# Kernel optimization log

Hardware: AMD Instinct MI355X
Metric: run time of the kernel (lower is better)

## Reference

```python
import jax, jax.numpy as jnp
import numpy as np
from jax import lax

B, N, D, E, P, K, H = 32, 512, 512, 8, 96, 25, 4
PAD = 12  # conv padding so length is preserved


def setup_inputs() -> dict:
    key = jax.random.key(0)
    ks = jax.random.split(key, 16)
    s = 0.05  # weight scale to keep softmax/cosine well-conditioned
    x = jax.random.normal(ks[0], (B, N, D), dtype=jnp.float32)
    router = jax.random.normal(ks[1], (1, E, D), dtype=jnp.float32)
    Wq = jax.random.normal(ks[2], (D, D), dtype=jnp.float32) * s
    bq = jax.random.normal(ks[3], (D,), dtype=jnp.float32) * s
    Wk = jax.random.normal(ks[4], (D, D), dtype=jnp.float32) * s
    bk = jax.random.normal(ks[5], (D,), dtype=jnp.float32) * s
    Wv = jax.random.normal(ks[6], (D, D), dtype=jnp.float32) * s
    bv = jax.random.normal(ks[7], (D,), dtype=jnp.float32) * s
    Wo = jax.random.normal(ks[8], (D, D), dtype=jnp.float32) * s
    bo = jax.random.normal(ks[9], (D,), dtype=jnp.float32) * s
    Wc = jax.random.normal(ks[10], (E, 2, K), dtype=jnp.float32) * s  # E experts' Conv1d(2,1,25) stacked as out-channels
    bc = jax.random.normal(ks[11], (E,), dtype=jnp.float32) * s
    Wp = jax.random.normal(ks[12], (E, D, P), dtype=jnp.float32) * s  # E experts' Linear(D,P), stored (in,out)
    bp = jax.random.normal(ks[13], (E, P), dtype=jnp.float32) * s
    return {"x": x, "router": router, "Wq": Wq, "bq": bq, "Wk": Wk, "bk": bk,
            "Wv": Wv, "bv": bv, "Wo": Wo, "bo": bo, "Wc": Wc, "bc": bc,
            "Wp": Wp, "bp": bp}


def _forward(x, router, Wq, bq, Wk, bk, Wv, bv, Wo, bo, Wc, bc, Wp, bp):
    b, n, d = x.shape
    e = router.shape[1]
    dk = d // H
    r = jnp.broadcast_to(router, (b, e, d))
    # multi-head attention: queries=router slots, keys/values=x (dropout = identity at eval)
    q = (r @ Wq + bq).reshape(b, e, H, dk)
    k = (x @ Wk + bk).reshape(b, n, H, dk)
    v = (x @ Wv + bv).reshape(b, n, H, dk)
    scale = 1.0 / jnp.sqrt(jnp.asarray(dk, x.dtype))
    scores = jnp.einsum('blhe,bshe->bhls', q, k)  # [b,H,e,n]
    A = jax.nn.softmax(scale * scores, axis=-1)
    att = jnp.einsum('bhls,bshd->blhd', A, v).reshape(b, e, d)
    att = att @ Wo + bo  # [b,e,d]
    # cosine-similarity routing score, mapped to (1+pi)/2
    dot = jnp.einsum('bed,bnd->ben', att, x)
    norm_a = jnp.linalg.norm(att, axis=2, keepdims=True)          # [b,e,1]
    norm_x = jnp.linalg.norm(x, axis=2)[:, None, :]                # [b,1,n]
    score = (1.0 + dot / (norm_a * norm_x)) / 2.0                  # [b,e,n]
    idx = jnp.argmax(score, axis=1)                                # [b,n] expert per token
    z = jnp.take_along_axis(att, idx[:, :, None], axis=1)          # [b,n,d]
    result = jnp.stack([x, z], axis=-2).reshape(b * n, 2, d)       # [bn,2,d]
    # run all E expert convs at once (experts stacked as output channels)
    conv_out = lax.conv_general_dilated(
        result, Wc, window_strides=(1,), padding=[(PAD, PAD)],
        dimension_numbers=('NCH', 'OIH', 'NCH')) + bc[None, :, None]  # [bn,E,d]
    lin = jnp.einsum('nel,elp->nep', conv_out, Wp) + bp[None]         # [bn,E,P]
    flat_idx = idx.reshape(-1)
    out = jnp.take_along_axis(lin, flat_idx[:, None, None], axis=1)[:, 0, :]
    return out.reshape(b, n, P)


def reference(x, router, Wq, bq, Wk, bk, Wv, bv, Wo, bo, Wc, bc, Wp, bp):
    return _forward(x, router, Wq, bq, Wk, bk, Wv, bv, Wo, bo, Wc, bc, Wp, bp)
```

## Files before the change

### kernel.cpp

```cpp
#include <hip/hip_runtime.h>
#include <hip/hip_bf16.h>

#define B_ 32
#define N_ 512
#define D_ 512
#define E_ 8
#define P_ 96
#define KC 25
#define H_ 4
#define DK 128
#define HE 32
#define BN 16384

typedef short short8 __attribute__((ext_vector_type(8)));
typedef float f32x4 __attribute__((ext_vector_type(4)));

#define OCNT  4096
#define OS2   4352
#define OM    5120
#define OC    21504
#define OA    21536
#define OAP   545824
#define OATT  676896
#define OTOK  807968
#define OWEFF 939040
#define OZC   1332256
#define OUP   1356832
#define OA1   5551136

__device__ __forceinline__ float b2f(short s) {
  unsigned u = ((unsigned)(unsigned short)s) << 16;
  return __builtin_bit_cast(float, u);
}
__device__ __forceinline__ unsigned short f2b(float f) {
  return __builtin_bit_cast(unsigned short, __float2bfloat16(f));
}

__global__ __launch_bounds__(256) void k_head(const float* __restrict__ router,
        const float* __restrict__ Wq, const float* __restrict__ bq,
        const float* __restrict__ Wk, const float* __restrict__ bk,
        const float* __restrict__ Wp, const float* __restrict__ Wc,
        float* __restrict__ M, float* __restrict__ c,
        int* __restrict__ cnt, float* __restrict__ s2,
        __hip_bfloat16* __restrict__ weff) {
  __shared__ float sm[5824];
  int bid = blockIdx.x;
  int tid = threadIdx.x;
  if (bid < 64) {
    float* rs = sm;
    float* ps = sm + 512;
    float* qs = sm + 768;
    int he = bid >> 1, ch = bid & 1;
    int h = he >> 3, e = he & 7;
    for (int i = tid; i < 512; i += 256) rs[i] = router[e * D_ + i];
    __syncthreads();
    {
      int j = tid & 127, dh = tid >> 7;
      const float* wq = Wq + h * 128 + j;
      float acc = 0.f;
      for (int d = dh * 256; d < dh * 256 + 256; d += 4) {
        acc = fmaf(rs[d], wq[d * D_], acc);
        acc = fmaf(rs[d + 1], wq[(d + 1) * D_], acc);
        acc = fmaf(rs[d + 2], wq[(d + 2) * D_], acc);
        acc = fmaf(rs[d + 3], wq[(d + 3) * D_], acc);
      }
      ps[dh * 128 + j] = acc;
    }
    __syncthreads();
    if (tid < 128) qs[tid] = ps[tid] + ps[128 + tid] + bq[h * 128 + tid];
    __syncthreads();
    {
      int d0 = ch * 256 + tid;
      const float* wrow = Wk + d0 * D_ + h * 128;
      float acc = 0.f;
      for (int jj = 0; jj < 128; jj += 4) {
        float4 wv = *(const float4*)(wrow + jj);
        acc = fmaf(wv.x, qs[jj], acc);
        acc = fmaf(wv.y, qs[jj + 1], acc);
        acc = fmaf(wv.z, qs[jj + 2], acc);
        acc = fmaf(wv.w, qs[jj + 3], acc);
      }
      M[he * D_ + d0] = acc;
    }
    if (ch == 0 && tid < 64) {
      float s = qs[tid] * bk[h * 128 + tid] + qs[tid + 64] * bk[h * 128 + tid + 64];
#pragma unroll
      for (int off = 32; off; off >>= 1) s += __shfl_xor(s, off);
      if (tid == 0) c[he] = s;
    }
  } else if (bid < 192) {
    float* T = sm;
    float* wcs = sm + 5760;
    int eb = bid - 64;
    int e = eb >> 4, mc = eb & 15;
    int lo = mc * 32 - 12;
    for (int idx = tid; idx < 56 * 24; idx += 256) {
      int lp = idx / 24, p4 = (idx - lp * 24) * 4;
      int l = lo + lp;
      float4 v = {0.f, 0.f, 0.f, 0.f};
      if (l >= 0 && l < D_) v = *(const float4*)(Wp + (e * D_ + l) * P_ + p4);
      T[p4 * 60 + lp] = v.x; T[(p4 + 1) * 60 + lp] = v.y;
      T[(p4 + 2) * 60 + lp] = v.z; T[(p4 + 3) * 60 + lp] = v.w;
    }
    if (tid < 50) wcs[tid] = Wc[e * 2 * KC + tid];
    __syncthreads();
    int m = tid & 31, pg = tid >> 5;
#pragma unroll
    for (int j = 0; j < 2; ++j)
      for (int k2 = 0; k2 < 12; ++k2) {
        int p = pg * 12 + k2;
        float acc = 0.f;
#pragma unroll
        for (int k = 0; k < KC; ++k)
          acc = fmaf(wcs[j * 25 + k], T[p * 60 + m - k + 24], acc);
        weff[(((e * 2 + j) * P_ + p) << 9) + mc * 32 + m] = __float2bfloat16(acc);
      }
  } else {
    int e = bid - 192;
    if (bid == 192) cnt[tid] = 0;
    if (tid < 192) {
      int p = tid % 96, lg = tid / 96;
      float s = 0.f;
      const float* wp = Wp + e * D_ * P_ + p;
      for (int l = lg * 256; l < lg * 256 + 256; ++l) s += wp[l * P_];
      sm[lg * 96 + p] = s;
    }
    __syncthreads();
    if (tid < 96) s2[e * 96 + tid] = sm[tid] + sm[96 + tid];
  }
}

__global__ __launch_bounds__(128) void k_logits(const float* __restrict__ x,
        const float* __restrict__ M, float* __restrict__ A0,
        float* __restrict__ A1) {
  __shared__ float xs[64 * 132];
  __shared__ float Ms[32 * 132];
  int dh = blockIdx.x & 1;
  int nt8 = (blockIdx.x >> 1) & 7;
  int b = blockIdx.x >> 4;
  int tid = threadIdx.x;
  const float* xb = x + (b * N_ + nt8 * 64) * D_ + dh * 256;
  const float* Mb = M + dh * 256;
  float acc[4][4] = {{0.f}};
  for (int kc = 0; kc < 2; ++kc) {
    for (int idx = tid; idx < 2048; idx += 128) {
      int r = idx >> 5, c4 = (idx & 31) * 4;
      *(float4*)(xs + r * 132 + c4) = *(const float4*)(xb + r * D_ + kc * 128 + c4);
    }
    for (int idx = tid; idx < 1024; idx += 128) {
      int r = idx >> 5, c4 = (idx & 31) * 4;
      *(float4*)(Ms + r * 132 + c4) = *(const float4*)(Mb + r * D_ + kc * 128 + c4);
    }
    __syncthreads();
    int nt = tid & 15, ht = tid >> 4;
#pragma unroll 4
    for (int d4 = 0; d4 < 128; d4 += 4) {
      float4 xv[4], mv[4];
#pragma unroll
      for (int i = 0; i < 4; ++i)
        xv[i] = *(const float4*)(xs + (nt + 16 * i) * 132 + d4);
#pragma unroll
      for (int j = 0; j < 4; ++j)
        mv[j] = *(const float4*)(Ms + (ht + 8 * j) * 132 + d4);
#pragma unroll
      for (int i = 0; i < 4; ++i)
#pragma unroll
        for (int j = 0; j < 4; ++j) {
          float s = acc[i][j];
          s = fmaf(xv[i].x, mv[j].x, s);
          s = fmaf(xv[i].y, mv[j].y, s);
          s = fmaf(xv[i].z, mv[j].z, s);
          s = fmaf(xv[i].w, mv[j].w, s);
          acc[i][j] = s;
        }
    }
    __syncthreads();
  }
  int nt = tid & 15, ht = tid >> 4;
  float* Ad = dh ? A1 : A0;
#pragma unroll
  for (int j = 0; j < 4; ++j) {
    int he = ht + 8 * j;
#pragma unroll
    for (int i = 0; i < 4; ++i)
      Ad[(b * HE + he) * N_ + nt8 * 64 + nt + 16 * i] = acc[i][j];
  }
}

__global__ __launch_bounds__(512) void k_usm(const float* __restrict__ x,
        const float* __restrict__ A0, const float* __restrict__ A1,
        const float* __restrict__ c, float* __restrict__ up) {
  __shared__ float V[32 * 520];
  __shared__ float As[64 * 33];
  __shared__ float inv_s[32];
  int nq = blockIdx.x, b = blockIdx.y;
  int tid = threadIdx.x;
  const float scale = 0.08838834764831845f;
  for (int idx = tid; idx < 32 * 128; idx += 512) {
    int he = idx >> 7, n4 = (idx & 127) * 4;
    float4 a0 = *(const float4*)(A0 + (b * HE + he) * N_ + n4);
    float4 a1 = *(const float4*)(A1 + (b * HE + he) * N_ + n4);
    float cc = c[he];
    float4 v;
    v.x = scale * (a0.x + a1.x + cc);
    v.y = scale * (a0.y + a1.y + cc);
    v.z = scale * (a0.z + a1.z + cc);
    v.w = scale * (a0.w + a1.w + cc);
    *(float4*)(V + he * 520 + n4) = v;
  }
  __syncthreads();
  {
    int w = tid >> 6, lane = tid & 63;
    int he = w * 4 + (lane >> 4);
    int l16 = lane & 15;
    float* vr = V + he * 520;
    float m = -1e30f;
    for (int n = l16; n < 512; n += 16) m = fmaxf(m, vr[n]);
    m = fmaxf(m, __shfl_xor(m, 1)); m = fmaxf(m, __shfl_xor(m, 2));
    m = fmaxf(m, __shfl_xor(m, 4)); m = fmaxf(m, __shfl_xor(m, 8));
    float s = 0.f;
    for (int n = l16; n < 512; n += 16) {
      float e = expf(vr[n] - m);
      vr[n] = e;
      s += e;
    }
    s += __shfl_xor(s, 1); s += __shfl_xor(s, 2);
    s += __shfl_xor(s, 4); s += __shfl_xor(s, 8);
    if (l16 == 0) inv_s[he] = 1.0f / s;
  }
  __syncthreads();
  for (int idx = tid; idx < 64 * 32; idx += 512) {
    int n = idx & 63, he = idx >> 6;
    As[n * 33 + he] = V[he * 520 + nq * 64 + n] * inv_s[he];
  }
  __syncthreads();
  int dq = tid & 127, hg = tid >> 7;
  const float* xb = x + (b * N_ + nq * 64) * D_ + dq * 4;
  float acc[8][4];
#pragma unroll
  for (int j = 0; j < 8; ++j)
#pragma unroll
    for (int k = 0; k < 4; ++k) acc[j][k] = 0.f;
  for (int n = 0; n < 64; ++n) {
    float4 xv = *(const float4*)(xb + n * D_);
    const float* ar = As + n * 33 + hg * 8;
#pragma unroll
    for (int j = 0; j < 8; ++j) {
      float a = ar[j];
      acc[j][0] = fmaf(a, xv.x, acc[j][0]);
      acc[j][1] = fmaf(a, xv.y, acc[j][1]);
      acc[j][2] = fmaf(a, xv.z, acc[j][2]);
      acc[j][3] = fmaf(a, xv.w, acc[j][3]);
    }
  }
  float* o = up + (((b * 8 + nq) * HE) + hg * 8) * D_ + dq * 4;
#pragma unroll
  for (int j = 0; j < 8; ++j) {
    float4 v; v.x = acc[j][0]; v.y = acc[j][1]; v.z = acc[j][2]; v.w = acc[j][3];
    *(float4*)(o + j * D_) = v;
  }
}

__global__ __launch_bounds__(256) void k_attpre(const float* __restrict__ up,
        const float* __restrict__ Wv, const float* __restrict__ bv,
        float* __restrict__ ap) {
  __shared__ float us[8 * D_];
  int e = blockIdx.x & 7;
  int ic = (blockIdx.x >> 3) & 3;
  int bq = blockIdx.x >> 5;
  for (int idx = threadIdx.x; idx < 8 * 128; idx += 256) {
    int rr = idx >> 7, d4 = (idx & 127) * 4;
    const float* base = up + (((bq * 8 + rr) * 8) * HE + ic * 8 + e) * D_ + d4;
    float4 s = {0.f, 0.f, 0.f, 0.f};
#pragma unroll
    for (int nq = 0; nq < 8; ++nq) {
      float4 v = *(const float4*)(base + nq * HE * D_);
      s.x += v.x; s.y += v.y; s.z += v.z; s.w += v.w;
    }
    *(float4*)(us + rr * D_ + d4) = s;
  }
  __syncthreads();
  int i = ic * 128 + (threadIdx.x & 127);
  int bg = threadIdx.x >> 7;
  const float* usb = us + bg * 4 * D_;
  float acc[4] = {0.f, 0.f, 0.f, 0.f};
  for (int d = 0; d < D_; d += 4) {
    float w0 = Wv[(d + 0) * D_ + i];
    float w1 = Wv[(d + 1) * D_ + i];
    float w2 = Wv[(d + 2) * D_ + i];
    float w3 = Wv[(d + 3) * D_ + i];
#pragma unroll
    for (int r = 0; r < 4; ++r) {
      float4 uv = *(const float4*)(usb + r * D_ + d);
      float s = acc[r];
      s = fmaf(uv.x, w0, s); s = fmaf(uv.y, w1, s);
      s = fmaf(uv.z, w2, s); s = fmaf(uv.w, w3, s);
      acc[r] = s;
    }
  }
  float bvi = bv[i];
#pragma unroll
  for (int r = 0; r < 4; ++r)
    ap[((bq * 8 + bg * 4 + r) * E_ + e) * D_ + i] = acc[r] + bvi;
}

__global__ __launch_bounds__(256) void k_att(const float* __restrict__ ap,
        const float* __restrict__ Wo, const float* __restrict__ bo,
        float* __restrict__ att) {
  __shared__ float ps[8 * D_];
  int b = blockIdx.x >> 2, oc = blockIdx.x & 3;
  for (int idx = threadIdx.x; idx < 8 * D_; idx += 256)
    ps[idx] = ap[b * E_ * D_ + idx];
  __syncthreads();
  int o = oc * 128 + (threadIdx.x & 127);
  int eg = threadIdx.x >> 7;
  const float* pe = ps + eg * 4 * D_;
  float acc[4] = {0.f, 0.f, 0.f, 0.f};
  for (int i2 = 0; i2 < D_; i2 += 4) {
    float w0 = Wo[(i2 + 0) * D_ + o];
    float w1 = Wo[(i2 + 1) * D_ + o];
    float w2 = Wo[(i2 + 2) * D_ + o];
    float w3 = Wo[(i2 + 3) * D_ + o];
#pragma unroll
    for (int r = 0; r < 4; ++r) {
      float4 pv = *(const float4*)(pe + r * D_ + i2);
      float s = acc[r];
      s = fmaf(pv.x, w0, s); s = fmaf(pv.y, w1, s);
      s = fmaf(pv.z, w2, s); s = fmaf(pv.w, w3, s);
      acc[r] = s;
    }
  }
  float boo = bo[o];
#pragma unroll
  for (int r = 0; r < 4; ++r)
    att[(b * E_ + eg * 4 + r) * D_ + o] = acc[r] + boo;
}

__global__ __launch_bounds__(256) void k_route2(const float* __restrict__ x,
        const float* __restrict__ att, const __hip_bfloat16* __restrict__ weff,
        const float* __restrict__ s2, const float* __restrict__ bc,
        const float* __restrict__ bp, int* __restrict__ cnt,
        int* __restrict__ tok, float* __restrict__ zc) {
  __shared__ float att_s[8 * D_];
  __shared__ float rn[8];
  __shared__ float red[4][520];
  __shared__ int blist[8][32];
  __shared__ int bcnt[8];
  int b = blockIdx.x >> 4, tile = blockIdx.x & 15;
  for (int idx = threadIdx.x; idx < 1024; idx += 256)
    *(float4*)(att_s + idx * 4) = *(const float4*)(att + b * E_ * D_ + idx * 4);
  if (threadIdx.x < 8) bcnt[threadIdx.x] = 0;
  __syncthreads();
  {
    int e = threadIdx.x >> 5, l = threadIdx.x & 31;
    float s = 0.f;
    for (int d0 = l; d0 < D_; d0 += 32) {
      float v = att_s[e * D_ + d0];
      s = fmaf(v, v, s);
    }
#pragma unroll
    for (int off = 16; off; off >>= 1) s += __shfl_xor(s, off);
    if (l == 0) rn[e] = 1.0f / sqrtf(s);
  }
  __syncthreads();
  int w = threadIdx.x >> 6, lane = threadIdx.x & 63;
  int e2 = lane & 7, ch = lane >> 3;
  float* rw = red[w];
  for (int i = 0; i < 8; ++i) {
    int t = b * N_ + tile * 32 + w * 8 + i;
    const float* xp = x + t * D_ + lane * 8;
    float4 xa = *(const float4*)xp;
    float4 xb4 = *(const float4*)(xp + 4);
    float p[8];
#pragma unroll
    for (int e = 0; e < 8; ++e) {
      const float* apt = att_s + e * D_ + lane * 8;
      float4 a0 = *(const float4*)apt;
      float4 a1 = *(const float4*)(apt + 4);
      float s = a0.x * xa.x;
      s = fmaf(a0.y, xa.y, s); s = fmaf(a0.z, xa.z, s); s = fmaf(a0.w, xa.w, s);
      s = fmaf(a1.x, xb4.x, s); s = fmaf(a1.y, xb4.y, s);
      s = fmaf(a1.z, xb4.z, s); s = fmaf(a1.w, xb4.w, s);
      p[e] = s;
    }
#pragma unroll
    for (int e = 0; e < 8; ++e) rw[e * 65 + lane] = p[e];
    float s = 0.f;
#pragma unroll
    for (int k = 0; k < 8; ++k) s += rw[e2 * 65 + ch * 8 + k];
    s += __shfl_xor(s, 8); s += __shfl_xor(s, 16); s += __shfl_xor(s, 32);
    float sc = s * rn[e2];
    int be = e2;
#pragma unroll
    for (int off = 1; off < 8; off <<= 1) {
      float o = __shfl_xor(sc, off);
      int oe = __shfl_xor(be, off);
      if (o > sc || (o == sc && oe < be)) { sc = o; be = oe; }
    }
    if (lane == 0) {
      int slot = atomicAdd(&bcnt[be], 1);
      blist[be][slot] = t;
    }
  }
  __syncthreads();
  {
    int e = threadIdx.x >> 5, r = threadIdx.x & 31;
    int ce = bcnt[e];
    int gs = 0;
    if (r == 0 && ce > 0) gs = atomicAdd(&cnt[e * 32], ce);
    gs = __shfl(gs, (threadIdx.x & 63) & 32);
    for (int k2 = r; k2 < ce; k2 += 32) tok[e * BN + gs + k2] = blist[e][k2];
  }
  int grp = threadIdx.x >> 4, l16 = threadIdx.x & 15;
  for (int r = 0; r < 3; ++r) {
    int P = tile * 48 + r * 16 + grp;
    int ez = P / 96, p = P - ez * 96;
    const short* wrow = (const short*)weff + (((ez * 2 + 1) * P_ + p) << 9);
    const float* arow = att_s + ez * D_;
    float acc = 0.f;
#pragma unroll
    for (int seg = 0; seg < 4; ++seg) {
      int d = seg * 128 + l16 * 8;
      short8 w8 = *(const short8*)(wrow + d);
      const float* a8 = arow + d;
      acc = fmaf(a8[0], b2f(w8[0]), acc); acc = fmaf(a8[1], b2f(w8[1]), acc);
      acc = fmaf(a8[2], b2f(w8[2]), acc); acc = fmaf(a8[3], b2f(w8[3]), acc);
      acc = fmaf(a8[4], b2f(w8[4]), acc); acc = fmaf(a8[5], b2f(w8[5]), acc);
      acc = fmaf(a8[6], b2f(w8[6]), acc); acc = fmaf(a8[7], b2f(w8[7]), acc);
    }
    acc += __shfl_xor(acc, 1); acc += __shfl_xor(acc, 2);
    acc += __shfl_xor(acc, 4); acc += __shfl_xor(acc, 8);
    if (l16 == 0)
      zc[(b * E_ + ez) * P_ + p] = acc + bc[ez] * s2[ez * 96 + p] + bp[ez * 96 + p];
  }
}

__global__ __launch_bounds__(256) void k_final(const float* __restrict__ x,
        const __hip_bfloat16* __restrict__ weff, const float* __restrict__ zc,
        const int* __restrict__ cnt, const int* __restrict__ tok,
        float* __restrict__ out) {
  __shared__ __align__(16) unsigned short xsb[32 * 520];
  __shared__ int toks[32];
  int g = blockIdx.x;
  int cl_e[E_], bs[E_ + 1];
  bs[0] = 0;
#pragma unroll
  for (int e = 0; e < E_; ++e) {
    cl_e[e] = cnt[e * 32];
    bs[e + 1] = bs[e] + ((cl_e[e] + 31) >> 5);
  }
  if (g >= bs[E_]) return;
  int e = 0;
#pragma unroll
  for (int k = 1; k < E_; ++k) if (g >= bs[k]) e = k;
  int base = (g - bs[e]) * 32;
  int cnt_e = cl_e[e];
  int cl = cnt_e - base; if (cl > 32) cl = 32;
  int tid = threadIdx.x;
  if (tid < 32) toks[tid] = (tid < cl) ? tok[e * BN + base + tid] : tok[e * BN + base];
  __syncthreads();
  for (int idx = tid; idx < 32 * 128; idx += 256) {
    int r = idx >> 7, c4 = (idx & 127) * 4;
    float4 v = *(const float4*)(x + toks[r] * D_ + c4);
    ushort4 u4;
    u4.x = f2b(v.x); u4.y = f2b(v.y); u4.z = f2b(v.z); u4.w = f2b(v.w);
    *(ushort4*)(xsb + r * 520 + c4) = u4;
  }
  __syncthreads();
  int wave = tid >> 6, lane = tid & 63;
  int mw = wave & 1, nw = wave >> 1;
  int m16 = lane & 15, quad = lane >> 4;
  const short* w0 = (const short*)(weff + (e * 2 + 0) * P_ * D_);
  f32x4 acc[3];
#pragma unroll
  for (int nt = 0; nt < 3; ++nt) acc[nt] = (f32x4){0.f, 0.f, 0.f, 0.f};
  const short* arow = (const short*)xsb + (mw * 16 + m16) * 520 + quad * 8;
  const short* brow = w0 + (nw * 48 + m16) * D_ + quad * 8;
  for (int kt = 0; kt < 16; ++kt) {
    int koff = kt * 32;
    short8 a = *(const short8*)(arow + koff);
#pragma unroll
    for (int nt = 0; nt < 3; ++nt) {
      short8 bf = *(const short8*)(brow + nt * 16 * D_ + koff);
      acc[nt] = __builtin_amdgcn_mfma_f32_16x16x32_bf16(a, bf, acc[nt], 0, 0, 0);
    }
  }
#pragma unroll
  for (int nt = 0; nt < 3; ++nt)
#pragma unroll
    for (int rr = 0; rr < 4; ++rr) {
      int row = mw * 16 + quad * 4 + rr;
      if (row < cl) {
        int tg = toks[row];
        int bb = tg >> 9;
        int p = nw * 48 + nt * 16 + m16;
        out[tg * P_ + p] = acc[nt][rr] + zc[(bb * E_ + e) * P_ + p];
      }
    }
}

extern "C" void kernel_launch(void* const* d_in, const int* in_sizes, int n_in,
                              void* d_out, int out_size, void* d_ws, size_t ws_size,
                              hipStream_t stream) {
  const float* x      = (const float*)d_in[0];
  const float* router = (const float*)d_in[1];
  const float* Wq     = (const float*)d_in[2];
  const float* bq     = (const float*)d_in[3];
  const float* Wk     = (const float*)d_in[4];
  const float* bk     = (const float*)d_in[5];
  const float* Wv     = (const float*)d_in[6];
  const float* bv     = (const float*)d_in[7];
  const float* Wo     = (const float*)d_in[8];
  const float* bo     = (const float*)d_in[9];
  const float* Wc     = (const float*)d_in[10];
  const float* bc     = (const float*)d_in[11];
  const float* Wp     = (const float*)d_in[12];
  const float* bp     = (const float*)d_in[13];
  float* out = (float*)d_out;
  float* w = (float*)d_ws;

  int*   cnt  = (int*)(w + OCNT);
  float* s2   = w + OS2;
  float* M    = w + OM;
  float* c    = w + OC;
  float* A0   = w + OA;
  float* A1   = w + OA1;
  float* ap   = w + OAP;
  float* att  = w + OATT;
  int*   tok  = (int*)(w + OTOK);
  __hip_bfloat16* weff = (__hip_bfloat16*)(w + OWEFF);
  float* zc   = w + OZC;
  float* up   = w + OUP;

  k_head<<<200, 256, 0, stream>>>(router, Wq, bq, Wk, bk, Wp, Wc, M, c, cnt, s2, weff);
  k_logits<<<512, 128, 0, stream>>>(x, M, A0, A1);
  k_usm<<<dim3(8, 32), 512, 0, stream>>>(x, A0, A1, c, up);
  k_attpre<<<128, 256, 0, stream>>>(up, Wv, bv, ap);
  k_att<<<128, 256, 0, stream>>>(ap, Wo, bo, att);
  k_route2<<<512, 256, 0, stream>>>(x, att, weff, s2, bc, bp, cnt, tok, zc);
  k_final<<<520, 256, 0, stream>>>(x, weff, zc, cnt, tok, out);
}
```

Baseline: 239.7 us.

## Fuse five downstream kernels into one cooperative kernel with grid syncs

Merges the softmax/value-pooling, value projection, output projection, routing, and expert MFMA stages into a single cooperative kernel of 256 blocks × 512 threads, with grid.sync() between stages. This removes four kernel launch gaps and the tail effects between dependent small kernels. In exchange, each stage is re-tiled to fit 256 blocks: the softmax runs in two halves to fit shared memory, the projections use one output per thread, routing packs two tiles per block, and the final stage loops over token groups with one wave idle. Grid-wide barriers and lower per-stage parallelism could offset the saved launch overhead.

```diff
diff --git a/kernel.cpp b/kernel.cpp
--- a/kernel.cpp
+++ b/kernel.cpp
@@ -1,5 +1,8 @@
 #include <hip/hip_runtime.h>
 #include <hip/hip_bf16.h>
+#include <hip/hip_cooperative_groups.h>
+
+namespace cg = cooperative_groups;
 
 #define B_ 32
 #define N_ 512
@@ -187,316 +190,314 @@
   }
 }
 
-__global__ __launch_bounds__(512) void k_usm(const float* __restrict__ x,
-        const float* __restrict__ A0, const float* __restrict__ A1,
-        const float* __restrict__ c, float* __restrict__ up) {
-  __shared__ float V[32 * 520];
-  __shared__ float As[64 * 33];
-  __shared__ float inv_s[32];
-  int nq = blockIdx.x, b = blockIdx.y;
-  int tid = threadIdx.x;
-  const float scale = 0.08838834764831845f;
-  for (int idx = tid; idx < 32 * 128; idx += 512) {
-    int he = idx >> 7, n4 = (idx & 127) * 4;
-    float4 a0 = *(const float4*)(A0 + (b * HE + he) * N_ + n4);
-    float4 a1 = *(const float4*)(A1 + (b * HE + he) * N_ + n4);
-    float cc = c[he];
-    float4 v;
-    v.x = scale * (a0.x + a1.x + cc);
-    v.y = scale * (a0.y + a1.y + cc);
-    v.z = scale * (a0.z + a1.z + cc);
-    v.w = scale * (a0.w + a1.w + cc);
-    *(float4*)(V + he * 520 + n4) = v;
-  }
-  __syncthreads();
+__global__ __launch_bounds__(512) void k_mega(
+        const float* __restrict__ x, const float* __restrict__ A0,
+        const float* __restrict__ A1, const float* __restrict__ c,
+        const float* __restrict__ Wv, const float* __restrict__ bv,
+        const float* __restrict__ Wo, const float* __restrict__ bo,
+        const __hip_bfloat16* __restrict__ weff, const float* __restrict__ s2,
+        const float* __restrict__ bc, const float* __restrict__ bp,
+        int* __restrict__ cnt, int* __restrict__ tok,
+        float* __restrict__ up, float* __restrict__ ap,
+        float* __restrict__ att, float* __restrict__ zc,
+        float* __restrict__ out) {
+  __shared__ float sm[12928];
+  cg::grid_group grid = cg::this_grid();
+  int blk = blockIdx.x, tid = threadIdx.x;
+
   {
-    int w = tid >> 6, lane = tid & 63;
-    int he = w * 4 + (lane >> 4);
-    int l16 = lane & 15;
-    float* vr = V + he * 520;
-    float m = -1e30f;
-    for (int n = l16; n < 512; n += 16) m = fmaxf(m, vr[n]);
-    m = fmaxf(m, __shfl_xor(m, 1)); m = fmaxf(m, __shfl_xor(m, 2));
-    m = fmaxf(m, __shfl_xor(m, 4)); m = fmaxf(m, __shfl_xor(m, 8));
-    float s = 0.f;
-    for (int n = l16; n < 512; n += 16) {
-      float e = expf(vr[n] - m);
-      vr[n] = e;
-      s += e;
-    }
-    s += __shfl_xor(s, 1); s += __shfl_xor(s, 2);
-    s += __shfl_xor(s, 4); s += __shfl_xor(s, 8);
-    if (l16 == 0) inv_s[he] = 1.0f / s;
-  }
-  __syncthreads();
-  for (int idx = tid; idx < 64 * 32; idx += 512) {
-    int n = idx & 63, he = idx >> 6;
-    As[n * 33 + he] = V[he * 520 + nq * 64 + n] * inv_s[he];
-  }
-  __syncthreads();
-  int dq = tid & 127, hg = tid >> 7;
-  const float* xb = x + (b * N_ + nq * 64) * D_ + dq * 4;
-  float acc[8][4];
-#pragma unroll
-  for (int j = 0; j < 8; ++j)
-#pragma unroll
-    for (int k = 0; k < 4; ++k) acc[j][k] = 0.f;
-  for (int n = 0; n < 64; ++n) {
-    float4 xv = *(const float4*)(xb + n * D_);
-    const float* ar = As + n * 33 + hg * 8;
+    float* V = sm;
+    float* As = sm + 8320;
+    float* inv_s = sm + 10432;
+    int nq = blk & 7, b = blk >> 3;
+    const float scale = 0.08838834764831845f;
+    for (int half = 0; half < 2; ++half) {
+      int he0 = half * 16;
+      for (int idx = tid; idx < 16 * 128; idx += 512) {
+        int hh = idx >> 7, n4 = (idx & 127) * 4;
+        int he = he0 + hh;
+        float4 a0 = *(const float4*)(A0 + (b * HE + he) * N_ + n4);
+        float4 a1 = *(const float4*)(A1 + (b * HE + he) * N_ + n4);
+        float cc = c[he];
+        float4 v;
+        v.x = scale * (a0.x + a1.x + cc);
+        v.y = scale * (a0.y + a1.y + cc);
+        v.z = scale * (a0.z + a1.z + cc);
+        v.w = scale * (a0.w + a1.w + cc);
+        *(float4*)(V + hh * 520 + n4) = v;
+      }
+      __syncthreads();
+      {
+        int w = tid >> 6, lane = tid & 63;
+        int hh = w * 2 + (lane >> 5);
+        int l32 = lane & 31;
+        float* vr = V + hh * 520;
+        float m = -1e30f;
+        for (int n = l32; n < 512; n += 32) m = fmaxf(m, vr[n]);
+        m = fmaxf(m, __shfl_xor(m, 1)); m = fmaxf(m, __shfl_xor(m, 2));
+        m = fmaxf(m, __shfl_xor(m, 4)); m = fmaxf(m, __shfl_xor(m, 8));
+        m = fmaxf(m, __shfl_xor(m, 16));
+        float ssum = 0.f;
+        for (int n = l32; n < 512; n += 32) {
+          float e2 = expf(vr[n] - m);
+          vr[n] = e2;
+          ssum += e2;
+        }
+        ssum += __shfl_xor(ssum, 1); ssum += __shfl_xor(ssum, 2);
+        ssum += __shfl_xor(ssum, 4); ssum += __shfl_xor(ssum, 8);
+        ssum += __shfl_xor(ssum, 16);
+        if (l32 == 0) inv_s[he0 + hh] = 1.0f / ssum;
+      }
+      __syncthreads();
+      for (int idx = tid; idx < 64 * 16; idx += 512) {
+        int n = idx & 63, hh = idx >> 6;
+        As[n * 33 + he0 + hh] = V[hh * 520 + nq * 64 + n] * inv_s[he0 + hh];
+      }
+      __syncthreads();
+    }
+    int dq = tid & 127, hg = tid >> 7;
+    const float* xb = x + (b * N_ + nq * 64) * D_ + dq * 4;
+    float acc[8][4];
+#pragma unroll
+    for (int j = 0; j < 8; ++j)
+#pragma unroll
+      for (int k = 0; k < 4; ++k) acc[j][k] = 0.f;
+    for (int n = 0; n < 64; ++n) {
+      float4 xv = *(const float4*)(xb + n * D_);
+      const float* ar = As + n * 33 + hg * 8;
+#pragma unroll
+      for (int j = 0; j < 8; ++j) {
+        float a = ar[j];
+        acc[j][0] = fmaf(a, xv.x, acc[j][0]);
+        acc[j][1] = fmaf(a, xv.y, acc[j][1]);
+        acc[j][2] = fmaf(a, xv.z, acc[j][2]);
+        acc[j][3] = fmaf(a, xv.w, acc[j][3]);
+      }
+    }
+    float* o = up + (((b * 8 + nq) * HE) + hg * 8) * D_ + dq * 4;
 #pragma unroll
     for (int j = 0; j < 8; ++j) {
-      float a = ar[j];
-      acc[j][0] = fmaf(a, xv.x, acc[j][0]);
-      acc[j][1] = fmaf(a, xv.y, acc[j][1]);
-      acc[j][2] = fmaf(a, xv.z, acc[j][2]);
-      acc[j][3] = fmaf(a, xv.w, acc[j][3]);
-    }
-  }
-  float* o = up + (((b * 8 + nq) * HE) + hg * 8) * D_ + dq * 4;
-#pragma unroll
-  for (int j = 0; j < 8; ++j) {
-    float4 v; v.x = acc[j][0]; v.y = acc[j][1]; v.z = acc[j][2]; v.w = acc[j][3];
-    *(float4*)(o + j * D_) = v;
-  }
-}
-
-__global__ __launch_bounds__(256) void k_attpre(const float* __restrict__ up,
-        const float* __restrict__ Wv, const float* __restrict__ bv,
-        float* __restrict__ ap) {
-  __shared__ float us[8 * D_];
-  int e = blockIdx.x & 7;
-  int ic = (blockIdx.x >> 3) & 3;
-  int bq = blockIdx.x >> 5;
-  for (int idx = threadIdx.x; idx < 8 * 128; idx += 256) {
-    int rr = idx >> 7, d4 = (idx & 127) * 4;
-    const float* base = up + (((bq * 8 + rr) * 8) * HE + ic * 8 + e) * D_ + d4;
-    float4 s = {0.f, 0.f, 0.f, 0.f};
-#pragma unroll
-    for (int nq = 0; nq < 8; ++nq) {
-      float4 v = *(const float4*)(base + nq * HE * D_);
-      s.x += v.x; s.y += v.y; s.z += v.z; s.w += v.w;
-    }
-    *(float4*)(us + rr * D_ + d4) = s;
-  }
-  __syncthreads();
-  int i = ic * 128 + (threadIdx.x & 127);
-  int bg = threadIdx.x >> 7;
-  const float* usb = us + bg * 4 * D_;
-  float acc[4] = {0.f, 0.f, 0.f, 0.f};
-  for (int d = 0; d < D_; d += 4) {
-    float w0 = Wv[(d + 0) * D_ + i];
-    float w1 = Wv[(d + 1) * D_ + i];
-    float w2 = Wv[(d + 2) * D_ + i];
-    float w3 = Wv[(d + 3) * D_ + i];
-#pragma unroll
-    for (int r = 0; r < 4; ++r) {
-      float4 uv = *(const float4*)(usb + r * D_ + d);
-      float s = acc[r];
-      s = fmaf(uv.x, w0, s); s = fmaf(uv.y, w1, s);
-      s = fmaf(uv.z, w2, s); s = fmaf(uv.w, w3, s);
-      acc[r] = s;
-    }
-  }
-  float bvi = bv[i];
-#pragma unroll
-  for (int r = 0; r < 4; ++r)
-    ap[((bq * 8 + bg * 4 + r) * E_ + e) * D_ + i] = acc[r] + bvi;
-}
-
-__global__ __launch_bounds__(256) void k_att(const float* __restrict__ ap,
-        const float* __restrict__ Wo, const float* __restrict__ bo,
-        float* __restrict__ att) {
-  __shared__ float ps[8 * D_];
-  int b = blockIdx.x >> 2, oc = blockIdx.x & 3;
-  for (int idx = threadIdx.x; idx < 8 * D_; idx += 256)
-    ps[idx] = ap[b * E_ * D_ + idx];
-  __syncthreads();
-  int o = oc * 128 + (threadIdx.x & 127);
-  int eg = threadIdx.x >> 7;
-  const float* pe = ps + eg * 4 * D_;
-  float acc[4] = {0.f, 0.f, 0.f, 0.f};
-  for (int i2 = 0; i2 < D_; i2 += 4) {
-    float w0 = Wo[(i2 + 0) * D_ + o];
-    float w1 = Wo[(i2 + 1) * D_ + o];
-    float w2 = Wo[(i2 + 2) * D_ + o];
-    float w3 = Wo[(i2 + 3) * D_ + o];
-#pragma unroll
-    for (int r = 0; r < 4; ++r) {
-      float4 pv = *(const float4*)(pe + r * D_ + i2);
-      float s = acc[r];
-      s = fmaf(pv.x, w0, s); s = fmaf(pv.y, w1, s);
-      s = fmaf(pv.z, w2, s); s = fmaf(pv.w, w3, s);
-      acc[r] = s;
-    }
-  }
-  float boo = bo[o];
-#pragma unroll
-  for (int r = 0; r < 4; ++r)
-    att[(b * E_ + eg * 4 + r) * D_ + o] = acc[r] + boo;
-}
-
-__global__ __launch_bounds__(256) void k_route2(const float* __restrict__ x,
-        const float* __restrict__ att, const __hip_bfloat16* __restrict__ weff,
-        const float* __restrict__ s2, const float* __restrict__ bc,
-        const float* __restrict__ bp, int* __restrict__ cnt,
-        int* __restrict__ tok, float* __restrict__ zc) {
-  __shared__ float att_s[8 * D_];
-  __shared__ float rn[8];
-  __shared__ float red[4][520];
-  __shared__ int blist[8][32];
-  __shared__ int bcnt[8];
-  int b = blockIdx.x >> 4, tile = blockIdx.x & 15;
-  for (int idx = threadIdx.x; idx < 1024; idx += 256)
-    *(float4*)(att_s + idx * 4) = *(const float4*)(att + b * E_ * D_ + idx * 4);
-  if (threadIdx.x < 8) bcnt[threadIdx.x] = 0;
-  __syncthreads();
+      float4 v; v.x = acc[j][0]; v.y = acc[j][1]; v.z = acc[j][2]; v.w = acc[j][3];
+      *(float4*)(o + j * D_) = v;
+    }
+  }
+  grid.sync();
+
   {
-    int e = threadIdx.x >> 5, l = threadIdx.x & 31;
-    float s = 0.f;
-    for (int d0 = l; d0 < D_; d0 += 32) {
-      float v = att_s[e * D_ + d0];
-      s = fmaf(v, v, s);
-    }
-#pragma unroll
-    for (int off = 16; off; off >>= 1) s += __shfl_xor(s, off);
-    if (l == 0) rn[e] = 1.0f / sqrtf(s);
-  }
-  __syncthreads();
-  int w = threadIdx.x >> 6, lane = threadIdx.x & 63;
-  int e2 = lane & 7, ch = lane >> 3;
-  float* rw = red[w];
-  for (int i = 0; i < 8; ++i) {
-    int t = b * N_ + tile * 32 + w * 8 + i;
-    const float* xp = x + t * D_ + lane * 8;
-    float4 xa = *(const float4*)xp;
-    float4 xb4 = *(const float4*)(xp + 4);
-    float p[8];
-#pragma unroll
-    for (int e = 0; e < 8; ++e) {
-      const float* apt = att_s + e * D_ + lane * 8;
-      float4 a0 = *(const float4*)apt;
-      float4 a1 = *(const float4*)(apt + 4);
-      float s = a0.x * xa.x;
-      s = fmaf(a0.y, xa.y, s); s = fmaf(a0.z, xa.z, s); s = fmaf(a0.w, xa.w, s);
-      s = fmaf(a1.x, xb4.x, s); s = fmaf(a1.y, xb4.y, s);
-      s = fmaf(a1.z, xb4.z, s); s = fmaf(a1.w, xb4.w, s);
-      p[e] = s;
-    }
-#pragma unroll
-    for (int e = 0; e < 8; ++e) rw[e * 65 + lane] = p[e];
-    float s = 0.f;
-#pragma unroll
-    for (int k = 0; k < 8; ++k) s += rw[e2 * 65 + ch * 8 + k];
-    s += __shfl_xor(s, 8); s += __shfl_xor(s, 16); s += __shfl_xor(s, 32);
-    float sc = s * rn[e2];
-    int be = e2;
-#pragma unroll
-    for (int off = 1; off < 8; off <<= 1) {
-      float o = __shfl_xor(sc, off);
-      int oe = __shfl_xor(be, off);
-      if (o > sc || (o == sc && oe < be)) { sc = o; be = oe; }
-    }
-    if (lane == 0) {
-      int slot = atomicAdd(&bcnt[be], 1);
-      blist[be][slot] = t;
-    }
-  }
-  __syncthreads();
+    float* us = sm;
+    int e = blk & 7, bq = (blk >> 3) & 3, ic64 = blk >> 5;
+    int he = (ic64 >> 1) * 8 + e;
+    for (int idx = tid; idx < 8 * 128; idx += 512) {
+      int rr = idx >> 7, d4 = (idx & 127) * 4;
+      const float* base_ = up + (((bq * 8 + rr) * 8) * HE + he) * D_ + d4;
+      float4 s4 = {0.f, 0.f, 0.f, 0.f};
+#pragma unroll
+      for (int nq2 = 0; nq2 < 8; ++nq2) {
+        float4 v = *(const float4*)(base_ + nq2 * HE * D_);
+        s4.x += v.x; s4.y += v.y; s4.z += v.z; s4.w += v.w;
+      }
+      *(float4*)(us + rr * 512 + d4) = s4;
+    }
+    __syncthreads();
+    int lane = tid & 63, bg = tid >> 6;
+    int i = ic64 * 64 + lane;
+    const float* ur = us + bg * 512;
+    float acc = 0.f;
+    for (int d = 0; d < 512; d += 4) {
+      float4 uv = *(const float4*)(ur + d);
+      acc = fmaf(uv.x, Wv[(d + 0) * D_ + i], acc);
+      acc = fmaf(uv.y, Wv[(d + 1) * D_ + i], acc);
+      acc = fmaf(uv.z, Wv[(d + 2) * D_ + i], acc);
+      acc = fmaf(uv.w, Wv[(d + 3) * D_ + i], acc);
+    }
+    ap[((bq * 8 + bg) * E_ + e) * D_ + i] = acc + bv[i];
+  }
+  grid.sync();
+
   {
-    int e = threadIdx.x >> 5, r = threadIdx.x & 31;
-    int ce = bcnt[e];
-    int gs = 0;
-    if (r == 0 && ce > 0) gs = atomicAdd(&cnt[e * 32], ce);
-    gs = __shfl(gs, (threadIdx.x & 63) & 32);
-    for (int k2 = r; k2 < ce; k2 += 32) tok[e * BN + gs + k2] = blist[e][k2];
-  }
-  int grp = threadIdx.x >> 4, l16 = threadIdx.x & 15;
-  for (int r = 0; r < 3; ++r) {
-    int P = tile * 48 + r * 16 + grp;
-    int ez = P / 96, p = P - ez * 96;
-    const short* wrow = (const short*)weff + (((ez * 2 + 1) * P_ + p) << 9);
-    const float* arow = att_s + ez * D_;
+    float* ps = sm;
+    int b = blk >> 3, oc64 = blk & 7;
+    for (int idx = tid; idx < 1024; idx += 512)
+      *(float4*)(ps + idx * 4) = *(const float4*)(ap + b * E_ * D_ + idx * 4);
+    __syncthreads();
+    int lane = tid & 63, eg = tid >> 6;
+    int o = oc64 * 64 + lane;
+    const float* pr = ps + eg * 512;
     float acc = 0.f;
-#pragma unroll
-    for (int seg = 0; seg < 4; ++seg) {
-      int d = seg * 128 + l16 * 8;
-      short8 w8 = *(const short8*)(wrow + d);
-      const float* a8 = arow + d;
-      acc = fmaf(a8[0], b2f(w8[0]), acc); acc = fmaf(a8[1], b2f(w8[1]), acc);
-      acc = fmaf(a8[2], b2f(w8[2]), acc); acc = fmaf(a8[3], b2f(w8[3]), acc);
-      acc = fmaf(a8[4], b2f(w8[4]), acc); acc = fmaf(a8[5], b2f(w8[5]), acc);
-      acc = fmaf(a8[6], b2f(w8[6]), acc); acc = fmaf(a8[7], b2f(w8[7]), acc);
-    }
-    acc += __shfl_xor(acc, 1); acc += __shfl_xor(acc, 2);
-    acc += __shfl_xor(acc, 4); acc += __shfl_xor(acc, 8);
-    if (l16 == 0)
-      zc[(b * E_ + ez) * P_ + p] = acc + bc[ez] * s2[ez * 96 + p] + bp[ez * 96 + p];
-  }
-}
-
-__global__ __launch_bounds__(256) void k_final(const float* __restrict__ x,
-        const __hip_bfloat16* __restrict__ weff, const float* __restrict__ zc,
-        const int* __restrict__ cnt, const int* __restrict__ tok,
-        float* __restrict__ out) {
-  __shared__ __align__(16) unsigned short xsb[32 * 520];
-  __shared__ int toks[32];
-  int g = blockIdx.x;
-  int cl_e[E_], bs[E_ + 1];
-  bs[0] = 0;
-#pragma unroll
-  for (int e = 0; e < E_; ++e) {
-    cl_e[e] = cnt[e * 32];
-    bs[e + 1] = bs[e] + ((cl_e[e] + 31) >> 5);
-  }
-  if (g >= bs[E_]) return;
-  int e = 0;
-#pragma unroll
-  for (int k = 1; k < E_; ++k) if (g >= bs[k]) e = k;
-  int base = (g - bs[e]) * 32;
-  int cnt_e = cl_e[e];
-  int cl = cnt_e - base; if (cl > 32) cl = 32;
-  int tid = threadIdx.x;
-  if (tid < 32) toks[tid] = (tid < cl) ? tok[e * BN + base + tid] : tok[e * BN + base];
-  __syncthreads();
-  for (int idx = tid; idx < 32 * 128; idx += 256) {
-    int r = idx >> 7, c4 = (idx & 127) * 4;
-    float4 v = *(const float4*)(x + toks[r] * D_ + c4);
-    ushort4 u4;
-    u4.x = f2b(v.x); u4.y = f2b(v.y); u4.z = f2b(v.z); u4.w = f2b(v.w);
-    *(ushort4*)(xsb + r * 520 + c4) = u4;
-  }
-  __syncthreads();
-  int wave = tid >> 6, lane = tid & 63;
-  int mw = wave & 1, nw = wave >> 1;
-  int m16 = lane & 15, quad = lane >> 4;
-  const short* w0 = (const short*)(weff + (e * 2 + 0) * P_ * D_);
-  f32x4 acc[3];
-#pragma unroll
-  for (int nt = 0; nt < 3; ++nt) acc[nt] = (f32x4){0.f, 0.f, 0.f, 0.f};
-  const short* arow = (const short*)xsb + (mw * 16 + m16) * 520 + quad * 8;
-  const short* brow = w0 + (nw * 48 + m16) * D_ + quad * 8;
-  for (int kt = 0; kt < 16; ++kt) {
-    int koff = kt * 32;
-    short8 a = *(const short8*)(arow + koff);
-#pragma unroll
-    for (int nt = 0; nt < 3; ++nt) {
-      short8 bf = *(const short8*)(brow + nt * 16 * D_ + koff);
-      acc[nt] = __builtin_amdgcn_mfma_f32_16x16x32_bf16(a, bf, acc[nt], 0, 0, 0);
-    }
-  }
-#pragma unroll
-  for (int nt = 0; nt < 3; ++nt)
-#pragma unroll
-    for (int rr = 0; rr < 4; ++rr) {
-      int row = mw * 16 + quad * 4 + rr;
-      if (row < cl) {
-        int tg = toks[row];
-        int bb = tg >> 9;
-        int p = nw * 48 + nt * 16 + m16;
-        out[tg * P_ + p] = acc[nt][rr] + zc[(bb * E_ + e) * P_ + p];
-      }
-    }
+    for (int i = 0; i < 512; i += 4) {
+      float4 pv = *(const float4*)(pr + i);
+      acc = fmaf(pv.x, Wo[(i + 0) * D_ + o], acc);
+      acc = fmaf(pv.y, Wo[(i + 1) * D_ + o], acc);
+      acc = fmaf(pv.z, Wo[(i + 2) * D_ + o], acc);
+      acc = fmaf(pv.w, Wo[(i + 3) * D_ + o], acc);
+    }
+    att[(b * E_ + eg) * D_ + o] = acc + bo[o];
+  }
+  grid.sync();
+
+  {
+    int s = tid >> 8, t = tid & 255;
+    float* base = sm + s * 6464;
+    float* att_s = base;
+    float* rn = base + 4096;
+    float* red = base + 4104;
+    int* blist = (int*)(base + 6184);
+    int* bcnt = (int*)(base + 6440);
+    int j = blk * 2 + s;
+    int b = j >> 4, tile = j & 15;
+    for (int idx = t; idx < 1024; idx += 256)
+      *(float4*)(att_s + idx * 4) = *(const float4*)(att + b * E_ * D_ + idx * 4);
+    if (t < 8) bcnt[t] = 0;
+    __syncthreads();
+    {
+      int e = t >> 5, l = t & 31;
+      float ss = 0.f;
+      for (int d0 = l; d0 < D_; d0 += 32) {
+        float v = att_s[e * D_ + d0];
+        ss = fmaf(v, v, ss);
+      }
+#pragma unroll
+      for (int off = 16; off; off >>= 1) ss += __shfl_xor(ss, off);
+      if (l == 0) rn[e] = 1.0f / sqrtf(ss);
+    }
+    __syncthreads();
+    int w = t >> 6, lane = t & 63;
+    int e2 = lane & 7, ch = lane >> 3;
+    float* rw = red + w * 520;
+    for (int i = 0; i < 8; ++i) {
+      int tg = b * N_ + tile * 32 + w * 8 + i;
+      const float* xp = x + tg * D_ + lane * 8;
+      float4 xa = *(const float4*)xp;
+      float4 xb4 = *(const float4*)(xp + 4);
+      float p[8];
+#pragma unroll
+      for (int e = 0; e < 8; ++e) {
+        const float* apt = att_s + e * D_ + lane * 8;
+        float4 a0 = *(const float4*)apt;
+        float4 a1 = *(const float4*)(apt + 4);
+        float ss = a0.x * xa.x;
+        ss = fmaf(a0.y, xa.y, ss); ss = fmaf(a0.z, xa.z, ss); ss = fmaf(a0.w, xa.w, ss);
+        ss = fmaf(a1.x, xb4.x, ss); ss = fmaf(a1.y, xb4.y, ss);
+        ss = fmaf(a1.z, xb4.z, ss); ss = fmaf(a1.w, xb4.w, ss);
+        p[e] = ss;
+      }
+#pragma unroll
+      for (int e = 0; e < 8; ++e) rw[e * 65 + lane] = p[e];
+      float ss = 0.f;
+#pragma unroll
+      for (int k = 0; k < 8; ++k) ss += rw[e2 * 65 + ch * 8 + k];
+      ss += __shfl_xor(ss, 8); ss += __shfl_xor(ss, 16); ss += __shfl_xor(ss, 32);
+      float sc = ss * rn[e2];
+      int be = e2;
+#pragma unroll
+      for (int off = 1; off < 8; off <<= 1) {
+        float o = __shfl_xor(sc, off);
+        int oe = __shfl_xor(be, off);
+        if (o > sc || (o == sc && oe < be)) { sc = o; be = oe; }
+      }
+      if (lane == 0) {
+        int slot = atomicAdd(&bcnt[be], 1);
+        blist[be * 32 + slot] = tg;
+      }
+    }
+    __syncthreads();
+    {
+      int e = t >> 5, r = t & 31;
+      int ce = bcnt[e];
+      int gs = 0;
+      if (r == 0 && ce > 0) gs = atomicAdd(&cnt[e * 32], ce);
+      gs = __shfl(gs, (t & 63) & 32);
+      for (int k2 = r; k2 < ce; k2 += 32) tok[e * BN + gs + k2] = blist[e * 32 + k2];
+    }
+    int grp = t >> 4, l16 = t & 15;
+    for (int r = 0; r < 3; ++r) {
+      int P = tile * 48 + r * 16 + grp;
+      int ez = P / 96, p = P - ez * 96;
+      const short* wrow = (const short*)weff + (((ez * 2 + 1) * P_ + p) << 9);
+      const float* arow = att_s + ez * D_;
+      float acc = 0.f;
+#pragma unroll
+      for (int seg = 0; seg < 4; ++seg) {
+        int d = seg * 128 + l16 * 8;
+        short8 w8 = *(const short8*)(wrow + d);
+        const float* a8 = arow + d;
+        acc = fmaf(a8[0], b2f(w8[0]), acc); acc = fmaf(a8[1], b2f(w8[1]), acc);
+        acc = fmaf(a8[2], b2f(w8[2]), acc); acc = fmaf(a8[3], b2f(w8[3]), acc);
+        acc = fmaf(a8[4], b2f(w8[4]), acc); acc = fmaf(a8[5], b2f(w8[5]), acc);
+        acc = fmaf(a8[6], b2f(w8[6]), acc); acc = fmaf(a8[7], b2f(w8[7]), acc);
+      }
+      acc += __shfl_xor(acc, 1); acc += __shfl_xor(acc, 2);
+      acc += __shfl_xor(acc, 4); acc += __shfl_xor(acc, 8);
+      if (l16 == 0)
+        zc[(b * E_ + ez) * P_ + p] = acc + bc[ez] * s2[ez * 96 + p] + bp[ez * 96 + p];
+    }
+  }
+  grid.sync();
+
+  {
+    unsigned short* xsb = (unsigned short*)sm;
+    int* toks = (int*)(sm + 8320);
+    int cl_e[E_], bsx[E_ + 1];
+    bsx[0] = 0;
+#pragma unroll
+    for (int e = 0; e < E_; ++e) {
+      cl_e[e] = cnt[e * 32];
+      bsx[e + 1] = bsx[e] + ((cl_e[e] + 31) >> 5);
+    }
+    int total = bsx[E_];
+    int niter = (total + 255) >> 8;
+    for (int it = 0; it < niter; ++it) {
+      int g = it * 256 + blk;
+      int e = 0, cl = 0, base_ = 0;
+      bool active = (g < total);
+      if (active) {
+#pragma unroll
+        for (int k = 1; k < E_; ++k) if (g >= bsx[k]) e = k;
+        base_ = (g - bsx[e]) * 32;
+        cl = cl_e[e] - base_; if (cl > 32) cl = 32;
+      }
+      if (tid < 32)
+        toks[tid] = active ? tok[e * BN + base_ + ((tid < cl) ? tid : 0)] : 0;
+      __syncthreads();
+      for (int idx = tid; idx < 32 * 128; idx += 512) {
+        int r = idx >> 7, c4 = (idx & 127) * 4;
+        float4 v = *(const float4*)(x + toks[r] * D_ + c4);
+        ushort4 u4;
+        u4.x = f2b(v.x); u4.y = f2b(v.y); u4.z = f2b(v.z); u4.w = f2b(v.w);
+        *(ushort4*)(xsb + r * 520 + c4) = u4;
+      }
+      __syncthreads();
+      int wave = tid >> 6, lane = tid & 63;
+      int mw = wave & 1, nw = wave >> 1;
+      int m16 = lane & 15, quad = lane >> 4;
+      if (nw < 3 && active) {
+        const short* w0 = (const short*)(weff + (e * 2 + 0) * P_ * D_);
+        f32x4 acc0 = {0.f, 0.f, 0.f, 0.f}, acc1 = {0.f, 0.f, 0.f, 0.f};
+        const short* arow = (const short*)xsb + (mw * 16 + m16) * 520 + quad * 8;
+        const short* brow = w0 + (nw * 32 + m16) * D_ + quad * 8;
+        for (int kt = 0; kt < 16; ++kt) {
+          int koff = kt * 32;
+          short8 a = *(const short8*)(arow + koff);
+          short8 b0 = *(const short8*)(brow + koff);
+          short8 b1 = *(const short8*)(brow + 16 * D_ + koff);
+          acc0 = __builtin_amdgcn_mfma_f32_16x16x32_bf16(a, b0, acc0, 0, 0, 0);
+          acc1 = __builtin_amdgcn_mfma_f32_16x16x32_bf16(a, b1, acc1, 0, 0, 0);
+        }
+#pragma unroll
+        for (int rr = 0; rr < 4; ++rr) {
+          int row = mw * 16 + quad * 4 + rr;
+          if (row < cl) {
+            int tg = toks[row];
+            int bb = tg >> 9;
+            int p0 = nw * 32 + m16;
+            out[tg * P_ + p0] = acc0[rr] + zc[(bb * E_ + e) * P_ + p0];
+            out[tg * P_ + p0 + 16] = acc1[rr] + zc[(bb * E_ + e) * P_ + p0 + 16];
+          }
+        }
+      }
+      __syncthreads();
+    }
+  }
 }
 
 extern "C" void kernel_launch(void* const* d_in, const int* in_sizes, int n_in,
@@ -534,9 +535,12 @@
 
   k_head<<<200, 256, 0, stream>>>(router, Wq, bq, Wk, bk, Wp, Wc, M, c, cnt, s2, weff);
   k_logits<<<512, 128, 0, stream>>>(x, M, A0, A1);
-  k_usm<<<dim3(8, 32), 512, 0, stream>>>(x, A0, A1, c, up);
-  k_attpre<<<128, 256, 0, stream>>>(up, Wv, bv, ap);
-  k_att<<<128, 256, 0, stream>>>(ap, Wo, bo, att);
-  k_route2<<<512, 256, 0, stream>>>(x, att, weff, s2, bc, bp, cnt, tok, zc);
-  k_final<<<520, 256, 0, stream>>>(x, weff, zc, cnt, tok, out);
+
+  void* kargs[] = {(void*)&x, (void*)&A0, (void*)&A1, (void*)&c,
+                   (void*)&Wv, (void*)&bv, (void*)&Wo, (void*)&bo,
+                   (void*)&weff, (void*)&s2, (void*)&bc, (void*)&bp,
+                   (void*)&cnt, (void*)&tok, (void*)&up, (void*)&ap,
+                   (void*)&att, (void*)&zc, (void*)&out};
+  hipLaunchCooperativeKernel((const void*)k_mega, dim3(256), dim3(512),
+                             kargs, 0, stream);
 }
```

Result: slower. 378.9 us (+58.1%).
